# Optimization experiments

Measured on AMD Instinct MI355X. Metric: run time of the kernel, lower is better.

## Reference

```python
import jax, jax.numpy as jnp
import numpy as np

B, D, H, W, C = 2, 160, 160, 160, 3


def _grid(d, h, w, dtype=jnp.float32):
    # identity coordinate grid, shape [d, h, w, 3]
    gx, gy, gz = jnp.meshgrid(jnp.arange(d, dtype=dtype),
                              jnp.arange(h, dtype=dtype),
                              jnp.arange(w, dtype=dtype), indexing='ij')
    return jnp.stack([gx, gy, gz], axis=-1)


def _trilinear(vol, loc):
    """Trilinear sample vol [D,H,W,C] at float coords loc [D,H,W,3] (border-clipped)."""
    d, h, w, c = vol.shape
    sizes = jnp.array([d, h, w], dtype=loc.dtype)
    loc = jnp.clip(loc, 0.0, sizes - 1.0)
    loc0 = jnp.floor(loc)
    wgt = loc - loc0                                   # fractional part, [D,H,W,3]
    i0 = loc0.astype(jnp.int32)
    i1 = jnp.minimum(i0 + 1, jnp.array([d - 1, h - 1, w - 1], dtype=jnp.int32))
    vol_flat = vol.reshape(-1, c)                      # [D*H*W, C]

    def flat(ix, iy, iz):
        return (ix * h + iy) * w + iz

    out = jnp.zeros(loc.shape[:-1] + (c,), dtype=vol.dtype)
    for bx in (0, 1):
        ix = i0[..., 0] if bx == 0 else i1[..., 0]
        wx = (1.0 - wgt[..., 0]) if bx == 0 else wgt[..., 0]
        for by in (0, 1):
            iy = i0[..., 1] if by == 0 else i1[..., 1]
            wy = (1.0 - wgt[..., 1]) if by == 0 else wgt[..., 1]
            for bz in (0, 1):
                iz = i0[..., 2] if bz == 0 else i1[..., 2]
                wz = (1.0 - wgt[..., 2]) if bz == 0 else wgt[..., 2]
                corner = jnp.take(vol_flat, flat(ix, iy, iz), axis=0)
                out = out + corner * (wx * wy * wz)[..., None]
    return out


def setup_inputs() -> dict:
    key = jax.random.key(0)
    k1, k2 = jax.random.split(key)
    warp1 = jax.random.normal(k1, (B, D, H, W, C), dtype=jnp.float32)
    warp2 = jax.random.normal(k2, (B, D, H, W, C), dtype=jnp.float32)
    return {"warp1": warp1, "warp2": warp2}


def reference(warp1, warp2):
    # Compose dense transforms applied in order [warp1, warp2]:
    #   u(x) = u2(x) + u1(x + u2(x))   (trilinear resample of u1)
    grid = _grid(D, H, W, dtype=warp1.dtype)

    def compose_pair(u1, u2):
        return u2 + _trilinear(u1, grid + u2)

    return jax.vmap(compose_pair)(warp1, warp2)
```

## Files before the change

kernel.cpp:

```cpp
#include <hip/hip_runtime.h>

constexpr int Bn = 2;
constexpr int Dn = 160;
constexpr int Hn = 160;
constexpr int Wn = 160;
constexpr int NV  = Bn * Dn * Hn * Wn;
constexpr int VOL = Dn * Hn * Wn;

constexpr int TPB  = 256;
constexpr int NBLK = NV / TPB;
constexpr int NXCD = 8;
constexpr int CHUNK = NBLK / NXCD;

__global__ __launch_bounds__(TPB) void compose_transform_kernel(
    const float* __restrict__ warp1,
    const float* __restrict__ warp2,
    float* __restrict__ out) {

    int bid = blockIdx.x;
    int swz = (bid & (NXCD - 1)) * CHUNK + (bid >> 3);

    int idx = swz * TPB + (int)threadIdx.x;

    int w  = idx % Wn;
    int t  = idx / Wn;
    int h  = t % Hn;
    t      = t / Hn;
    int d  = t % Dn;
    int b  = t / Dn;

    int base3 = idx * 3;
    float u2x = __builtin_nontemporal_load(warp2 + base3 + 0);
    float u2y = __builtin_nontemporal_load(warp2 + base3 + 1);
    float u2z = __builtin_nontemporal_load(warp2 + base3 + 2);

    float lx = fminf(fmaxf((float)d + u2x, 0.0f), (float)(Dn - 1));
    float ly = fminf(fmaxf((float)h + u2y, 0.0f), (float)(Hn - 1));
    float lz = fminf(fmaxf((float)w + u2z, 0.0f), (float)(Wn - 1));

    int ixb = min((int)floorf(lx), Dn - 2);
    int iyb = min((int)floorf(ly), Hn - 2);
    int izb = min((int)floorf(lz), Wn - 2);

    float wx1 = lx - (float)ixb, wx0 = 1.0f - wx1;
    float wy1 = ly - (float)iyb, wy0 = 1.0f - wy1;
    float wz1 = lz - (float)izb, wz0 = 1.0f - wz1;

    const float* __restrict__ u1 = warp1 + b * (VOL * 3);

    const float* p00 = u1 + ((ixb * Hn + iyb) * Wn + izb) * 3;
    const float* p01 = p00 + Wn * 3;
    const float* p10 = p00 + Hn * Wn * 3;
    const float* p11 = p10 + Wn * 3;

    float a00_0 = p00[0], a00_1 = p00[1], a00_2 = p00[2];
    float a00_3 = p00[3], a00_4 = p00[4], a00_5 = p00[5];
    float a01_0 = p01[0], a01_1 = p01[1], a01_2 = p01[2];
    float a01_3 = p01[3], a01_4 = p01[4], a01_5 = p01[5];
    float a10_0 = p10[0], a10_1 = p10[1], a10_2 = p10[2];
    float a10_3 = p10[3], a10_4 = p10[4], a10_5 = p10[5];
    float a11_0 = p11[0], a11_1 = p11[1], a11_2 = p11[2];
    float a11_3 = p11[3], a11_4 = p11[4], a11_5 = p11[5];

    float w00 = wx0 * wy0;
    float w01 = wx0 * wy1;
    float w10 = wx1 * wy0;
    float w11 = wx1 * wy1;

    float rx, ry, rz;
    float accx, accy, accz;

    rx = fmaf(wz1, a00_3, wz0 * a00_0);
    ry = fmaf(wz1, a00_4, wz0 * a00_1);
    rz = fmaf(wz1, a00_5, wz0 * a00_2);
    accx = w00 * rx; accy = w00 * ry; accz = w00 * rz;

    rx = fmaf(wz1, a01_3, wz0 * a01_0);
    ry = fmaf(wz1, a01_4, wz0 * a01_1);
    rz = fmaf(wz1, a01_5, wz0 * a01_2);
    accx = fmaf(w01, rx, accx); accy = fmaf(w01, ry, accy); accz = fmaf(w01, rz, accz);

    rx = fmaf(wz1, a10_3, wz0 * a10_0);
    ry = fmaf(wz1, a10_4, wz0 * a10_1);
    rz = fmaf(wz1, a10_5, wz0 * a10_2);
    accx = fmaf(w10, rx, accx); accy = fmaf(w10, ry, accy); accz = fmaf(w10, rz, accz);

    rx = fmaf(wz1, a11_3, wz0 * a11_0);
    ry = fmaf(wz1, a11_4, wz0 * a11_1);
    rz = fmaf(wz1, a11_5, wz0 * a11_2);
    accx = fmaf(w11, rx, accx); accy = fmaf(w11, ry, accy); accz = fmaf(w11, rz, accz);

    __builtin_nontemporal_store(u2x + accx, out + base3 + 0);
    __builtin_nontemporal_store(u2y + accy, out + base3 + 1);
    __builtin_nontemporal_store(u2z + accz, out + base3 + 2);
}

extern "C" void kernel_launch(void* const* d_in, const int* in_sizes, int n_in,
                              void* d_out, int out_size, void* d_ws, size_t ws_size,
                              hipStream_t stream) {
    const float* warp1 = (const float*)d_in[0];
    const float* warp2 = (const float*)d_in[1];
    float* out = (float*)d_out;

    compose_transform_kernel<<<NBLK, TPB, 0, stream>>>(warp1, warp2, out);
}
```

Before: 345.1 us.

## Stage 3D halo tile of warp1 in LDS via direct global-to-LDS loads

Each block now handles an 8x8x8 output tile with two voxels per thread. It first copies a 16^3 halo region of warp1 into shared memory using global_load_lds, then serves trilinear gathers from LDS when the corner cube falls inside the halo, and falls back to global loads otherwise. The aim is to replace scattered global gathers with reuse from LDS. In exchange each block loads roughly 8x redundant halo data, needs about 49KB of LDS per block, which limits occupancy, and adds a block-wide barrier.

```diff
diff --git a/kernel.cpp b/kernel.cpp
--- a/kernel.cpp
+++ b/kernel.cpp
@@ -1,98 +1,168 @@
 #include <hip/hip_runtime.h>
 
-constexpr int Bn = 2;
-constexpr int Dn = 160;
-constexpr int Hn = 160;
-constexpr int Wn = 160;
-constexpr int NV  = Bn * Dn * Hn * Wn;
+constexpr int Bn = 2, Dn = 160, Hn = 160, Wn = 160;
 constexpr int VOL = Dn * Hn * Wn;
+constexpr int NV  = Bn * VOL;
 
-constexpr int TPB  = 256;
-constexpr int NBLK = NV / TPB;
+constexpr int Td = 8, Th = 8, Tw = 8;
+constexpr int TPB = 256;
+constexpr int NTd = Dn / Td, NTh = Hn / Th, NTw = Wn / Tw;
+constexpr int TILES = Bn * NTd * NTh * NTw;
+constexpr int HALO = 4;
+constexpr int SP    = Td + 2 * HALO;
+constexpr int SROW  = SP * 3 + 1;
+constexpr int SLICE = SP * SROW;
+constexpr int SDW   = SP * SLICE;
+constexpr int NIT   = SDW / TPB;
 constexpr int NXCD = 8;
-constexpr int CHUNK = NBLK / NXCD;
+constexpr int CHUNK = TILES / NXCD;
+
+typedef const __attribute__((address_space(1))) unsigned int* gas1_t;
+typedef __attribute__((address_space(3))) unsigned int* las3_t;
 
 __global__ __launch_bounds__(TPB) void compose_transform_kernel(
     const float* __restrict__ warp1,
     const float* __restrict__ warp2,
     float* __restrict__ out) {
 
+    __shared__ float lds[SDW];
+
     int bid = blockIdx.x;
     int swz = (bid & (NXCD - 1)) * CHUNK + (bid >> 3);
 
-    int idx = swz * TPB + (int)threadIdx.x;
+    int wt = swz % NTw; int t = swz / NTw;
+    int ht = t % NTh;   t /= NTh;
+    int dt = t % NTd;   int b = t / NTd;
+    int d0 = dt * Td, h0 = ht * Th, w0 = wt * Tw;
+    int dB = d0 - HALO, hB = h0 - HALO, wB = w0 - HALO;
 
-    int w  = idx % Wn;
-    int t  = idx / Wn;
-    int h  = t % Hn;
-    t      = t / Hn;
-    int d  = t % Dn;
-    int b  = t / Dn;
+    const float* __restrict__ u1 = warp1 + (size_t)b * (VOL * 3);
+    int tid = (int)threadIdx.x;
 
-    int base3 = idx * 3;
-    float u2x = __builtin_nontemporal_load(warp2 + base3 + 0);
-    float u2y = __builtin_nontemporal_load(warp2 + base3 + 1);
-    float u2z = __builtin_nontemporal_load(warp2 + base3 + 2);
+    {
+        int r  = tid / SROW;
+        int k  = tid - r * SROW;
+        int dd = r >> 4;
+        int hh = r & 15;
+        int wbase = tid & ~63;
+#pragma unroll 7
+        for (int it = 0; it < NIT; ++it) {
+            int wv = (k * 43) >> 7;
+            int c  = k - wv * 3;
+            int sd = min(max(dB + dd, 0), Dn - 1);
+            int sh = min(max(hB + hh, 0), Hn - 1);
+            int sw = min(max(wB + wv, 0), Wn - 1);
+            int gdw = ((sd * Hn + sh) * Wn + sw) * 3 + c;
+            __builtin_amdgcn_global_load_lds(
+                (gas1_t)(const unsigned int*)(u1 + gdw),
+                (las3_t)((unsigned int*)lds + (wbase + (it << 8))),
+                4, 0, 0);
+            k += 11; hh += 5;
+            if (k >= SROW) { k -= SROW; hh += 1; }
+            if (hh >= SP)  { hh -= SP;  dd += 1; }
+        }
+    }
 
-    float lx = fminf(fmaxf((float)d + u2x, 0.0f), (float)(Dn - 1));
-    float ly = fminf(fmaxf((float)h + u2y, 0.0f), (float)(Hn - 1));
-    float lz = fminf(fmaxf((float)w + u2z, 0.0f), (float)(Wn - 1));
+    int   ixbA, iybA, izbA, idxA;  bool inbA;
+    float wz0A, wz1A, w00A, w01A, w10A, w11A, u2xA, u2yA, u2zA;
+    int   ixbB, iybB, izbB, idxB;  bool inbB;
+    float wz0B, wz1B, w00B, w01B, w10B, w11B, u2xB, u2yB, u2zB;
 
-    int ixb = min((int)floorf(lx), Dn - 2);
-    int iyb = min((int)floorf(ly), Hn - 2);
-    int izb = min((int)floorf(lz), Wn - 2);
+#define PRE(SUF, V)                                                          \
+    {                                                                        \
+        int v = (V);                                                         \
+        int ow = v & 7, oh = (v >> 3) & 7, od = v >> 6;                      \
+        int d = d0 + od, h = h0 + oh, w = w0 + ow;                           \
+        idx##SUF = ((b * Dn + d) * Hn + h) * Wn + w;                         \
+        int base3 = idx##SUF * 3;                                            \
+        u2x##SUF = __builtin_nontemporal_load(warp2 + base3 + 0);            \
+        u2y##SUF = __builtin_nontemporal_load(warp2 + base3 + 1);            \
+        u2z##SUF = __builtin_nontemporal_load(warp2 + base3 + 2);            \
+        float lx = fminf(fmaxf((float)d + u2x##SUF, 0.0f), (float)(Dn - 1)); \
+        float ly = fminf(fmaxf((float)h + u2y##SUF, 0.0f), (float)(Hn - 1)); \
+        float lz = fminf(fmaxf((float)w + u2z##SUF, 0.0f), (float)(Wn - 1)); \
+        ixb##SUF = min((int)floorf(lx), Dn - 2);                             \
+        iyb##SUF = min((int)floorf(ly), Hn - 2);                             \
+        izb##SUF = min((int)floorf(lz), Wn - 2);                             \
+        float wx1 = lx - (float)ixb##SUF, wx0 = 1.0f - wx1;                  \
+        float wy1 = ly - (float)iyb##SUF, wy0 = 1.0f - wy1;                  \
+        wz1##SUF = lz - (float)izb##SUF; wz0##SUF = 1.0f - wz1##SUF;         \
+        w00##SUF = wx0 * wy0; w01##SUF = wx0 * wy1;                          \
+        w10##SUF = wx1 * wy0; w11##SUF = wx1 * wy1;                          \
+        inb##SUF = (ixb##SUF >= dB) & (ixb##SUF <= dB + SP - 2) &            \
+                   (iyb##SUF >= hB) & (iyb##SUF <= hB + SP - 2) &            \
+                   (izb##SUF >= wB) & (izb##SUF <= wB + SP - 2);             \
+    }
 
-    float wx1 = lx - (float)ixb, wx0 = 1.0f - wx1;
-    float wy1 = ly - (float)iyb, wy0 = 1.0f - wy1;
-    float wz1 = lz - (float)izb, wz0 = 1.0f - wz1;
+    PRE(A, tid)
+    PRE(B, tid + TPB)
+#undef PRE
 
-    const float* __restrict__ u1 = warp1 + b * (VOL * 3);
+    __syncthreads();
 
-    const float* p00 = u1 + ((ixb * Hn + iyb) * Wn + izb) * 3;
-    const float* p01 = p00 + Wn * 3;
-    const float* p10 = p00 + Hn * Wn * 3;
-    const float* p11 = p10 + Wn * 3;
+#define RESOLVE(SUF)                                                         \
+    {                                                                        \
+        float a00_0, a00_1, a00_2, a00_3, a00_4, a00_5;                      \
+        float a01_0, a01_1, a01_2, a01_3, a01_4, a01_5;                      \
+        float a10_0, a10_1, a10_2, a10_3, a10_4, a10_5;                      \
+        float a11_0, a11_1, a11_2, a11_3, a11_4, a11_5;                      \
+        if (__builtin_expect(inb##SUF, 1)) {                                 \
+            const float* L = lds + ((ixb##SUF - dB) * SLICE +                \
+                                    (iyb##SUF - hB) * SROW +                 \
+                                    (izb##SUF - wB) * 3);                    \
+            a00_0 = L[0];         a00_1 = L[1];         a00_2 = L[2];        \
+            a00_3 = L[3];         a00_4 = L[4];         a00_5 = L[5];        \
+            a01_0 = L[SROW+0];    a01_1 = L[SROW+1];    a01_2 = L[SROW+2];   \
+            a01_3 = L[SROW+3];    a01_4 = L[SROW+4];    a01_5 = L[SROW+5];   \
+            a10_0 = L[SLICE+0];   a10_1 = L[SLICE+1];   a10_2 = L[SLICE+2];  \
+            a10_3 = L[SLICE+3];   a10_4 = L[SLICE+4];   a10_5 = L[SLICE+5];  \
+            a11_0 = L[SLICE+SROW+0]; a11_1 = L[SLICE+SROW+1];                \
+            a11_2 = L[SLICE+SROW+2]; a11_3 = L[SLICE+SROW+3];                \
+            a11_4 = L[SLICE+SROW+4]; a11_5 = L[SLICE+SROW+5];                \
+        } else {                                                             \
+            const float* p00 = u1 + ((ixb##SUF * Hn + iyb##SUF) * Wn +       \
+                                     izb##SUF) * 3;                          \
+            const float* p01 = p00 + Wn * 3;                                 \
+            const float* p10 = p00 + Hn * Wn * 3;                            \
+            const float* p11 = p10 + Wn * 3;                                 \
+            a00_0 = p00[0]; a00_1 = p00[1]; a00_2 = p00[2];                  \
+            a00_3 = p00[3]; a00_4 = p00[4]; a00_5 = p00[5];                  \
+            a01_0 = p01[0]; a01_1 = p01[1]; a01_2 = p01[2];                  \
+            a01_3 = p01[3]; a01_4 = p01[4]; a01_5 = p01[5];                  \
+            a10_0 = p10[0]; a10_1 = p10[1]; a10_2 = p10[2];                  \
+            a10_3 = p10[3]; a10_4 = p10[4]; a10_5 = p10[5];                  \
+            a11_0 = p11[0]; a11_1 = p11[1]; a11_2 = p11[2];                  \
+            a11_3 = p11[3]; a11_4 = p11[4]; a11_5 = p11[5];                  \
+        }                                                                    \
+        float rx, ry, rz, accx, accy, accz;                                  \
+        rx = fmaf(wz1##SUF, a00_3, wz0##SUF * a00_0);                        \
+        ry = fmaf(wz1##SUF, a00_4, wz0##SUF * a00_1);                        \
+        rz = fmaf(wz1##SUF, a00_5, wz0##SUF * a00_2);                        \
+        accx = w00##SUF * rx; accy = w00##SUF * ry; accz = w00##SUF * rz;    \
+        rx = fmaf(wz1##SUF, a01_3, wz0##SUF * a01_0);                        \
+        ry = fmaf(wz1##SUF, a01_4, wz0##SUF * a01_1);                        \
+        rz = fmaf(wz1##SUF, a01_5, wz0##SUF * a01_2);                        \
+        accx = fmaf(w01##SUF, rx, accx); accy = fmaf(w01##SUF, ry, accy);    \
+        accz = fmaf(w01##SUF, rz, accz);                                     \
+        rx = fmaf(wz1##SUF, a10_3, wz0##SUF * a10_0);                        \
+        ry = fmaf(wz1##SUF, a10_4, wz0##SUF * a10_1);                        \
+        rz = fmaf(wz1##SUF, a10_5, wz0##SUF * a10_2);                        \
+        accx = fmaf(w10##SUF, rx, accx); accy = fmaf(w10##SUF, ry, accy);    \
+        accz = fmaf(w10##SUF, rz, accz);                                     \
+        rx = fmaf(wz1##SUF, a11_3, wz0##SUF * a11_0);                        \
+        ry = fmaf(wz1##SUF, a11_4, wz0##SUF * a11_1);                        \
+        rz = fmaf(wz1##SUF, a11_5, wz0##SUF * a11_2);                        \
+        accx = fmaf(w11##SUF, rx, accx); accy = fmaf(w11##SUF, ry, accy);    \
+        accz = fmaf(w11##SUF, rz, accz);                                     \
+        int ob = idx##SUF * 3;                                               \
+        __builtin_nontemporal_store(u2x##SUF + accx, out + ob + 0);          \
+        __builtin_nontemporal_store(u2y##SUF + accy, out + ob + 1);          \
+        __builtin_nontemporal_store(u2z##SUF + accz, out + ob + 2);          \
+    }
 
-    float a00_0 = p00[0], a00_1 = p00[1], a00_2 = p00[2];
-    float a00_3 = p00[3], a00_4 = p00[4], a00_5 = p00[5];
-    float a01_0 = p01[0], a01_1 = p01[1], a01_2 = p01[2];
-    float a01_3 = p01[3], a01_4 = p01[4], a01_5 = p01[5];
-    float a10_0 = p10[0], a10_1 = p10[1], a10_2 = p10[2];
-    float a10_3 = p10[3], a10_4 = p10[4], a10_5 = p10[5];
-    float a11_0 = p11[0], a11_1 = p11[1], a11_2 = p11[2];
-    float a11_3 = p11[3], a11_4 = p11[4], a11_5 = p11[5];
-
-    float w00 = wx0 * wy0;
-    float w01 = wx0 * wy1;
-    float w10 = wx1 * wy0;
-    float w11 = wx1 * wy1;
-
-    float rx, ry, rz;
-    float accx, accy, accz;
-
-    rx = fmaf(wz1, a00_3, wz0 * a00_0);
-    ry = fmaf(wz1, a00_4, wz0 * a00_1);
-    rz = fmaf(wz1, a00_5, wz0 * a00_2);
-    accx = w00 * rx; accy = w00 * ry; accz = w00 * rz;
-
-    rx = fmaf(wz1, a01_3, wz0 * a01_0);
-    ry = fmaf(wz1, a01_4, wz0 * a01_1);
-    rz = fmaf(wz1, a01_5, wz0 * a01_2);
-    accx = fmaf(w01, rx, accx); accy = fmaf(w01, ry, accy); accz = fmaf(w01, rz, accz);
-
-    rx = fmaf(wz1, a10_3, wz0 * a10_0);
-    ry = fmaf(wz1, a10_4, wz0 * a10_1);
-    rz = fmaf(wz1, a10_5, wz0 * a10_2);
-    accx = fmaf(w10, rx, accx); accy = fmaf(w10, ry, accy); accz = fmaf(w10, rz, accz);
-
-    rx = fmaf(wz1, a11_3, wz0 * a11_0);
-    ry = fmaf(wz1, a11_4, wz0 * a11_1);
-    rz = fmaf(wz1, a11_5, wz0 * a11_2);
-    accx = fmaf(w11, rx, accx); accy = fmaf(w11, ry, accy); accz = fmaf(w11, rz, accz);
-
-    __builtin_nontemporal_store(u2x + accx, out + base3 + 0);
-    __builtin_nontemporal_store(u2y + accy, out + base3 + 1);
-    __builtin_nontemporal_store(u2z + accz, out + base3 + 2);
+    RESOLVE(A)
+    RESOLVE(B)
+#undef RESOLVE
 }
 
 extern "C" void kernel_launch(void* const* d_in, const int* in_sizes, int n_in,
@@ -102,5 +172,5 @@
     const float* warp2 = (const float*)d_in[1];
     float* out = (float*)d_out;
 
-    compose_transform_kernel<<<NBLK, TPB, 0, stream>>>(warp1, warp2, out);
+    compose_transform_kernel<<<TILES, TPB, 0, stream>>>(warp1, warp2, out);
 }
```

Measured after the change: 350.0 us. No clear change (+1.4%).
